# Kernel optimization log

Measured on AMD Instinct MI355X. Metric: run time of the kernel, lower is better.

## Reference

```python
import jax, jax.numpy as jnp
import numpy as np

D_MODEL = 1024
H = 16
D_K = D_MODEL // H
B, S = 1, 4096


def setup_inputs() -> dict:
    key = jax.random.key(0)
    ks = jax.random.split(key, 12)
    std = 1.0 / np.sqrt(D_MODEL)
    inp = {
        "q": jax.random.normal(ks[0], (B, S, D_MODEL), dtype=jnp.float32),
        "k": jax.random.normal(ks[1], (B, S, D_MODEL), dtype=jnp.float32),
        "v": jax.random.normal(ks[2], (B, S, D_MODEL), dtype=jnp.float32),
        "mask": jax.random.randint(ks[3], (B, 1, S, S), 0, 2).astype(bool),
        # nn.Linear params (torch convention: y = x @ W.T + b), weights [out, in]
        "wq": jax.random.uniform(ks[4], (D_MODEL, D_MODEL), jnp.float32, -std, std),
        "bq": jax.random.uniform(ks[5], (D_MODEL,), jnp.float32, -std, std),
        "wk": jax.random.uniform(ks[6], (D_MODEL, D_MODEL), jnp.float32, -std, std),
        "bk": jax.random.uniform(ks[7], (D_MODEL,), jnp.float32, -std, std),
        "wv": jax.random.uniform(ks[8], (D_MODEL, D_MODEL), jnp.float32, -std, std),
        "bv": jax.random.uniform(ks[9], (D_MODEL,), jnp.float32, -std, std),
        "wo": jax.random.uniform(ks[10], (D_MODEL, D_MODEL), jnp.float32, -std, std),
        "bo": jax.random.uniform(ks[11], (D_MODEL,), jnp.float32, -std, std),
    }
    return inp


def _split_heads(x):
    # [b, s, (h d)] -> [b, h, s, d]
    b, s, _ = x.shape
    return x.reshape(b, s, H, D_K).transpose(0, 2, 1, 3)


def reference(q, k, v, mask, wq, bq, wk, bk, wv, bv, wo, bo):
    b, s, d = q.shape
    qh = _split_heads(q @ wq.T + bq)
    kh = _split_heads(k @ wk.T + bk)
    vh = _split_heads(v @ wv.T + bv)
    # NOTE: original scales by sqrt(d_model), not sqrt(d_k) — keep faithful.
    score = jnp.einsum("bhqd,bhkd->bhqk", qh, kh) / jnp.sqrt(jnp.float32(d))
    score = jnp.where(mask, jnp.float32(-1e9), score)
    attn = jax.nn.softmax(score, axis=-1)  # dropout is identity in eval mode
    wv_out = jnp.einsum("bhqk,bhkd->bhqd", attn, vh)
    concat = wv_out.transpose(0, 2, 1, 3).reshape(b, s, d)
    return concat @ wo.T + bo
```

## Files before the change

### kernel.cpp

```cpp
#include <hip/hip_runtime.h>
#include <hip/hip_bf16.h>
#include <math.h>

typedef __attribute__((ext_vector_type(4))) float f32x4;
typedef __attribute__((ext_vector_type(8))) short s16x8;
typedef __attribute__((ext_vector_type(4))) short s16x4;

#define S_LEN 4096
#define DMODEL 1024
#define NHEADS 16
#define DHEAD 64

__device__ __forceinline__ unsigned short f2bf(float f) {
  union { float f; unsigned int u; } x; x.f = f;
  return (unsigned short)((x.u + 0x7FFFu + ((x.u >> 16) & 1u)) >> 16);
}

__device__ __forceinline__ float fexp2(float x) {
#if __has_builtin(__builtin_amdgcn_exp2f)
  return __builtin_amdgcn_exp2f(x);
#else
  float r; asm("v_exp_f32 %0, %1" : "=v"(r) : "v"(x)); return r;
#endif
}

__device__ __forceinline__ void gload_lds16(const void* g, void* l) {
  __builtin_amdgcn_global_load_lds(
      (const __attribute__((address_space(1))) unsigned int*)g,
      (__attribute__((address_space(3))) unsigned int*)l, 16, 0, 0);
}

__global__ __launch_bounds__(256) void mask_lane(const int* __restrict__ mask,
                                                 unsigned long long* __restrict__ lmask) {
  const int qg = blockIdx.x;
  const int wv = threadIdx.x >> 6, l = threadIdx.x & 63;
  const int lr = l & 15, lg = l >> 4;
  const int* base = mask + (size_t)(qg * 16 + lr) * S_LEN;
  for (int t = wv; t < 64; t += 4) {
#pragma unroll
    for (int kg = 0; kg < 4; ++kg) {
#pragma unroll
      for (int j = 0; j < 4; ++j) {
        unsigned long long b = __ballot(base[t * 64 + kg * 16 + lg * 4 + j] != 0);
        if (l == 0) lmask[((size_t)qg * 64 + t) * 16 + kg * 4 + j] = b;
      }
    }
  }
}

__global__ __launch_bounds__(256) void cast_bf16(
    const float* __restrict__ s0, const float* __restrict__ s1, const float* __restrict__ s2,
    const float* __restrict__ s3, const float* __restrict__ s4, const float* __restrict__ s5,
    const float* __restrict__ s6, unsigned short* __restrict__ dst) {
  const int z = blockIdx.y;
  const float* src = (z == 0) ? s0 : (z == 1) ? s1 : (z == 2) ? s2 :
                     (z == 3) ? s3 : (z == 4) ? s4 : (z == 5) ? s5 : s6;
  const int n = (z < 3) ? (S_LEN * DMODEL) : (DMODEL * DMODEL);
  unsigned short* d = dst + ((z < 3) ? (size_t)z * S_LEN * DMODEL
                                     : (size_t)3 * S_LEN * DMODEL + (size_t)(z - 3) * DMODEL * DMODEL);
  const int i = (blockIdx.x * 256 + threadIdx.x) * 4;
  if (i < n) {
    f32x4 v = *(const f32x4*)(src + i);
    s16x4 o;
#pragma unroll
    for (int j = 0; j < 4; ++j) o[j] = (short)f2bf(v[j]);
    *(s16x4*)(d + i) = o;
  }
}

template<int OUT_MODE>
__device__ __forceinline__ void gemm_b16_body(const unsigned short* __restrict__ A,
                                              const unsigned short* __restrict__ W,
                                              const float* __restrict__ bias,
                                              void* __restrict__ outp, float scale) {
  constexpr int K = DMODEL, N = DMODEL, M = S_LEN;
  constexpr int BM = 128, BK = 32;
  __shared__ unsigned short Alds[BM * BK];
  __shared__ unsigned short Blds[BM * BK];
  const int tid = threadIdx.x;
  const int l = tid & 63, wid = tid >> 6;
  const int lr = l & 15, lg = l >> 4;
  const int bm = blockIdx.x * BM, bn = blockIdx.y * BM;
  const int wm = (wid >> 1) * 64, wn = (wid & 1) * 64;

  const int srow = tid >> 2;
  const int schunk = (tid & 3) ^ (srow & 3);
  const unsigned short* As = A + (size_t)(bm + srow) * K + schunk * 8;
  const unsigned short* Ws = W + (size_t)(bn + srow) * K + schunk * 8;
  unsigned short* Ald = &Alds[srow * BK + (tid & 3) * 8];
  unsigned short* Bld = &Blds[srow * BK + (tid & 3) * 8];

  f32x4 acc[4][4] = {};
  const int xc = (lg ^ (lr & 3)) * 8;

  for (int k0 = 0; k0 < K; k0 += BK) {
    __syncthreads();
    gload_lds16(As + k0, Ald);
    gload_lds16(As + (size_t)64 * K + k0, Ald + 64 * BK);
    gload_lds16(Ws + k0, Bld);
    gload_lds16(Ws + (size_t)64 * K + k0, Bld + 64 * BK);
    __syncthreads();

    s16x8 af[4], bfr[4];
#pragma unroll
    for (int mi = 0; mi < 4; ++mi)
      af[mi] = *(const s16x8*)&Alds[(wm + mi * 16 + lr) * BK + xc];
#pragma unroll
    for (int ni = 0; ni < 4; ++ni)
      bfr[ni] = *(const s16x8*)&Blds[(wn + ni * 16 + lr) * BK + xc];
#pragma unroll
    for (int mi = 0; mi < 4; ++mi)
#pragma unroll
      for (int ni = 0; ni < 4; ++ni)
        acc[mi][ni] = __builtin_amdgcn_mfma_f32_16x16x32_bf16(af[mi], bfr[ni], acc[mi][ni], 0, 0, 0);
  }

#pragma unroll
  for (int ni = 0; ni < 4; ++ni) {
    const int n = bn + wn + ni * 16 + lr;
    const float bv = bias[n];
#pragma unroll
    for (int mi = 0; mi < 4; ++mi) {
#pragma unroll
      for (int j = 0; j < 4; ++j) {
        const int m = bm + wm + mi * 16 + lg * 4 + j;
        const float val = (acc[mi][ni][j] + bv) * scale;
        if constexpr (OUT_MODE == 1) {
          unsigned short* out = (unsigned short*)outp;
          out[((size_t)(n >> 6) * M + m) * DHEAD + (n & 63)] = f2bf(val);
        } else if constexpr (OUT_MODE == 2) {
          unsigned short* out = (unsigned short*)outp;
          out[((size_t)(n >> 6) * DHEAD + (n & 63)) * M + m] = f2bf(val);
        } else {
          float* out = (float*)outp;
          out[(size_t)m * N + n] = val;
        }
      }
    }
  }
}

template<int A_BF16, int OUT_MODE>
__device__ __forceinline__ void gemm_f32_body(const void* __restrict__ Ap,
                                              const float* __restrict__ W,
                                              const float* __restrict__ bias,
                                              void* __restrict__ outp, float scale) {
  constexpr int K = DMODEL, N = DMODEL, M = S_LEN;
  constexpr int BM = 128, BK = 32, LDT = 40;
  __shared__ unsigned short Alds[BM * LDT];
  __shared__ unsigned short Blds[BM * LDT];
  const int tid = threadIdx.x;
  const int l = tid & 63, wid = tid >> 6;
  const int lr = l & 15, lg = l >> 4;
  const int bm = blockIdx.x * BM;
  const int bn = blockIdx.y * BM;
  const int wm = (wid >> 1) * 64, wn = (wid & 1) * 64;

  f32x4 acc[4][4] = {};

  for (int k0 = 0; k0 < K; k0 += BK) {
    __syncthreads();
    if constexpr (A_BF16) {
      const unsigned short* A = (const unsigned short*)Ap;
      const int col = (tid & 3) * 8, row = tid >> 2;
#pragma unroll
      for (int p = 0; p < 2; ++p) {
        const int r = row + p * 64;
        *(s16x8*)&Alds[r * LDT + col] =
            *(const s16x8*)(A + (size_t)(bm + r) * K + k0 + col);
      }
    } else {
      const float* A = (const float*)Ap;
      const int col = (tid & 7) * 4, row = tid >> 3;
#pragma unroll
      for (int p = 0; p < 4; ++p) {
        const int r = row + p * 32;
        f32x4 vv = *(const f32x4*)(A + (size_t)(bm + r) * K + k0 + col);
        s16x4 o;
#pragma unroll
        for (int j = 0; j < 4; ++j) o[j] = (short)f2bf(vv[j]);
        *(s16x4*)&Alds[r * LDT + col] = o;
      }
    }
    {
      const float* Wf = W;
      const int col = (tid & 7) * 4, row = tid >> 3;
#pragma unroll
      for (int p = 0; p < 4; ++p) {
        const int r = row + p * 32;
        f32x4 vv = *(const f32x4*)(Wf + (size_t)(bn + r) * K + k0 + col);
        s16x4 o;
#pragma unroll
        for (int j = 0; j < 4; ++j) o[j] = (short)f2bf(vv[j]);
        *(s16x4*)&Blds[r * LDT + col] = o;
      }
    }
    __syncthreads();
    s16x8 af[4], bfr[4];
#pragma unroll
    for (int mi = 0; mi < 4; ++mi)
      af[mi] = *(const s16x8*)&Alds[(wm + mi * 16 + lr) * LDT + lg * 8];
#pragma unroll
    for (int ni = 0; ni < 4; ++ni)
      bfr[ni] = *(const s16x8*)&Blds[(wn + ni * 16 + lr) * LDT + lg * 8];
#pragma unroll
    for (int mi = 0; mi < 4; ++mi)
#pragma unroll
      for (int ni = 0; ni < 4; ++ni)
        acc[mi][ni] = __builtin_amdgcn_mfma_f32_16x16x32_bf16(af[mi], bfr[ni], acc[mi][ni], 0, 0, 0);
  }

#pragma unroll
  for (int ni = 0; ni < 4; ++ni) {
    const int n = bn + wn + ni * 16 + lr;
    const float bv = bias[n];
#pragma unroll
    for (int mi = 0; mi < 4; ++mi) {
#pragma unroll
      for (int j = 0; j < 4; ++j) {
        const int m = bm + wm + mi * 16 + lg * 4 + j;
        const float val = (acc[mi][ni][j] + bv) * scale;
        if constexpr (OUT_MODE == 1) {
          unsigned short* out = (unsigned short*)outp;
          out[((size_t)(n >> 6) * M + m) * DHEAD + (n & 63)] = f2bf(val);
        } else if constexpr (OUT_MODE == 2) {
          unsigned short* out = (unsigned short*)outp;
          out[((size_t)(n >> 6) * DHEAD + (n & 63)) * M + m] = f2bf(val);
        } else {
          float* out = (float*)outp;
          out[(size_t)m * N + n] = val;
        }
      }
    }
  }
}

#define QSCALE 0.04508422f

__global__ __launch_bounds__(256) void proj_qkv_b16(
    const unsigned short* __restrict__ qb, const unsigned short* __restrict__ kb,
    const unsigned short* __restrict__ vb,
    const unsigned short* __restrict__ wqb, const float* __restrict__ bq,
    const unsigned short* __restrict__ wkb, const float* __restrict__ bk,
    const unsigned short* __restrict__ wvb, const float* __restrict__ bv,
    unsigned short* __restrict__ ws) {
  const int z = blockIdx.z;
  if (z == 0)      gemm_b16_body<1>(qb, wqb, bq, ws, QSCALE);
  else if (z == 1) gemm_b16_body<1>(kb, wkb, bk, ws + (size_t)S_LEN * DMODEL, 1.0f);
  else             gemm_b16_body<2>(vb, wvb, bv, ws + (size_t)2 * S_LEN * DMODEL, 1.0f);
}
__global__ __launch_bounds__(256) void outproj_b16(
    const unsigned short* __restrict__ concat, const unsigned short* __restrict__ wob,
    const float* __restrict__ bo, float* __restrict__ out) {
  gemm_b16_body<0>(concat, wob, bo, out, 1.0f);
}
__global__ __launch_bounds__(256) void proj_qkv_f32(
    const float* __restrict__ q, const float* __restrict__ k, const float* __restrict__ v,
    const float* __restrict__ wq, const float* __restrict__ bq,
    const float* __restrict__ wk, const float* __restrict__ bk,
    const float* __restrict__ wv, const float* __restrict__ bv,
    unsigned short* __restrict__ ws) {
  const int z = blockIdx.z;
  if (z == 0)      gemm_f32_body<0, 1>(q, wq, bq, ws, QSCALE);
  else if (z == 1) gemm_f32_body<0, 1>(k, wk, bk, ws + (size_t)S_LEN * DMODEL, 1.0f);
  else             gemm_f32_body<0, 2>(v, wv, bv, ws + (size_t)2 * S_LEN * DMODEL, 1.0f);
}
__global__ __launch_bounds__(256) void outproj_f32(
    const unsigned short* __restrict__ concat, const float* __restrict__ wo,
    const float* __restrict__ bo, float* __restrict__ out) {
  gemm_f32_body<1, 0>(concat, wo, bo, out, 1.0f);
}

template<int NSPLIT>
__global__ __launch_bounds__(512, 4) void attn_fwd(
    const unsigned short* __restrict__ Qh, const unsigned short* __restrict__ Kh,
    const unsigned short* __restrict__ Vt, const unsigned long long* __restrict__ lmask,
    unsigned short* __restrict__ outp,
    float* __restrict__ lpart) {
  __shared__ unsigned short Klds[2][64 * 64];
  __shared__ unsigned short Vlds[2][64 * 64];
  __shared__ unsigned short P_lds[8][32][76];

  const int tid = threadIdx.x;
  const int l = tid & 63, wid = tid >> 6;
  const int lr = l & 15, lg = l >> 4;
  const int per = 32 * NSPLIT;
  const int swz = (blockIdx.x & 7) * per + (blockIdx.x >> 3);
  const int h = swz / (16 * NSPLIT);
  const int split = (NSPLIT == 2) ? ((swz >> 4) & 1) : 0;
  const int qb = swz & 15;
  const int qrow0 = qb * 256 + wid * 32;
  const int kv0 = split * (S_LEN / NSPLIT);
  constexpr int NT = (S_LEN / NSPLIT) / 64;
  const int T0 = kv0 >> 6;

  const unsigned short* Qbase = Qh + ((size_t)h * S_LEN + qrow0) * DHEAD;
  s16x8 qf[2][2];
#pragma unroll
  for (int sub = 0; sub < 2; ++sub)
#pragma unroll
    for (int ds = 0; ds < 2; ++ds)
      qf[sub][ds] = *(const s16x8*)(Qbase + (sub * 16 + lr) * DHEAD + ds * 32 + lg * 8);

  const int wid_u = __builtin_amdgcn_readfirstlane(wid);
  const int qg0 = qb * 16 + wid_u * 2;
  const unsigned long long* mq0 = lmask + (size_t)qg0 * 64 * 16;
  const unsigned long long* mq1 = mq0 + (size_t)64 * 16;

  const int srow = l >> 3;
  const int schunk = (l & 7) ^ srow;
  const unsigned short* Kst = Kh + (size_t)h * S_LEN * DHEAD
                              + (size_t)(kv0 + wid * 8 + srow) * DHEAD + schunk * 8;
  const unsigned short* Vst = Vt + (size_t)h * DHEAD * S_LEN
                              + (size_t)(wid * 8 + srow) * S_LEN + kv0 + schunk * 8;
  const int sdst = (wid * 8) * 64;

  f32x4 o_acc[2][4] = {};
  float lsum[2] = {0.f, 0.f};

  gload_lds16(Kst, &Klds[0][sdst]);
  gload_lds16(Vst, &Vlds[0][sdst]);
  __syncthreads();

  const int xr = lr & 7;

  for (int t = 0; t < NT; ++t) {
    const int buf = t & 1;
    if (t < NT - 1) {
      gload_lds16(Kst + (size_t)(t + 1) * 64 * DHEAD, &Klds[buf ^ 1][sdst]);
      gload_lds16(Vst + (t + 1) * 64, &Vlds[buf ^ 1][sdst]);
    }

    const unsigned short* Kb = &Klds[buf][0];
    f32x4 sc[2][4];
    __builtin_amdgcn_s_setprio(1);
#pragma unroll
    for (int kg = 0; kg < 4; ++kg) {
      const int r = kg * 16 + lr;
      s16x8 k0 = *(const s16x8*)(Kb + r * 64 + ((lg ^ xr) * 8));
      s16x8 k1 = *(const s16x8*)(Kb + r * 64 + (((lg + 4) ^ xr) * 8));
#pragma unroll
      for (int sub = 0; sub < 2; ++sub) {
        f32x4 z = {};
        z = __builtin_amdgcn_mfma_f32_16x16x32_bf16(k0, qf[sub][0], z, 0, 0, 0);
        sc[sub][kg] = __builtin_amdgcn_mfma_f32_16x16x32_bf16(k1, qf[sub][1], z, 0, 0, 0);
      }
    }
    __builtin_amdgcn_s_setprio(0);

    const size_t mo = (size_t)(T0 + t) * 16;
#pragma unroll
    for (int sub = 0; sub < 2; ++sub) {
      const unsigned long long* qp = (sub ? mq1 : mq0) + mo;
#pragma unroll
      for (int kg = 0; kg < 4; ++kg) {
        float p[4];
#pragma unroll
        for (int j = 0; j < 4; ++j) {
          const unsigned long long mw = qp[kg * 4 + j];
          float pv = fexp2(sc[sub][kg][j]);
          asm("v_cndmask_b32 %0, %1, 0, %2" : "=v"(pv) : "v"(pv), "s"(mw));
          p[j] = pv;
          lsum[sub] += pv;
        }
        unsigned int w0, w1;
        asm("v_cvt_pk_bf16_f32 %0, %1, %2" : "=v"(w0) : "v"(p[0]), "v"(p[1]));
        asm("v_cvt_pk_bf16_f32 %0, %1, %2" : "=v"(w1) : "v"(p[2]), "v"(p[3]));
        uint2 pk; pk.x = w0; pk.y = w1;
        *(uint2*)&P_lds[wid][sub * 16 + lr][kg * 16 + lg * 4] = pk;
      }
    }
    asm volatile("s_waitcnt lgkmcnt(0)" ::: "memory");
    __builtin_amdgcn_sched_barrier(0);

    s16x8 pf[2][2];
#pragma unroll
    for (int sub = 0; sub < 2; ++sub)
#pragma unroll
      for (int ks = 0; ks < 2; ++ks)
        pf[sub][ks] = *(const s16x8*)&P_lds[wid][sub * 16 + lr][ks * 32 + lg * 8];

    const unsigned short* Vb = &Vlds[buf][0];
    __builtin_amdgcn_s_setprio(1);
#pragma unroll
    for (int dg = 0; dg < 4; ++dg) {
      const int r = dg * 16 + lr;
      s16x8 v0 = *(const s16x8*)(Vb + r * 64 + ((lg ^ xr) * 8));
      s16x8 v1 = *(const s16x8*)(Vb + r * 64 + (((lg + 4) ^ xr) * 8));
#pragma unroll
      for (int sub = 0; sub < 2; ++sub) {
        o_acc[sub][dg] = __builtin_amdgcn_mfma_f32_16x16x32_bf16(pf[sub][0], v0, o_acc[sub][dg], 0, 0, 0);
        o_acc[sub][dg] = __builtin_amdgcn_mfma_f32_16x16x32_bf16(pf[sub][1], v1, o_acc[sub][dg], 0, 0, 0);
      }
    }
    __builtin_amdgcn_s_setprio(0);

    __syncthreads();
  }

#pragma unroll
  for (int sub = 0; sub < 2; ++sub) {
    lsum[sub] += __shfl_xor(lsum[sub], 16, 64);
    lsum[sub] += __shfl_xor(lsum[sub], 32, 64);
  }

  if constexpr (NSPLIT == 2) {
    unsigned short* op = outp + ((size_t)(split * NHEADS + h) * S_LEN) * DHEAD;
#pragma unroll
    for (int sub = 0; sub < 2; ++sub)
#pragma unroll
      for (int dg = 0; dg < 4; ++dg)
#pragma unroll
        for (int j = 0; j < 4; ++j) {
          const int q = qrow0 + sub * 16 + lg * 4 + j;
          op[(size_t)q * DHEAD + dg * 16 + lr] = f2bf(o_acc[sub][dg][j]);
        }
    if (l < 16) {
      float* lp = lpart + (size_t)(split * NHEADS + h) * S_LEN + qrow0;
      lp[lr] = lsum[0];
      lp[16 + lr] = lsum[1];
    }
  } else {
    float rs[2][4];
#pragma unroll
    for (int sub = 0; sub < 2; ++sub)
#pragma unroll
      for (int j = 0; j < 4; ++j)
        rs[sub][j] = __shfl(lsum[sub], lg * 4 + j, 64);
#pragma unroll
    for (int sub = 0; sub < 2; ++sub)
#pragma unroll
      for (int dg = 0; dg < 4; ++dg)
#pragma unroll
        for (int j = 0; j < 4; ++j) {
          const int q = qrow0 + sub * 16 + lg * 4 + j;
          outp[(size_t)q * DMODEL + h * DHEAD + dg * 16 + lr] =
              f2bf(o_acc[sub][dg][j] / rs[sub][j]);
        }
  }
}

__global__ __launch_bounds__(256) void attn_combine(
    const unsigned short* __restrict__ opart, const float* __restrict__ lpart,
    unsigned short* __restrict__ concat) {
  const int idx = blockIdx.x * 256 + threadIdx.x;
  const int d4 = (idx & 15) * 4;
  const int hq = idx >> 4;
  const int h = hq >> 12, q = hq & 4095;
  const size_t o0 = ((size_t)h * S_LEN + q) * DHEAD + d4;
  const size_t o1 = o0 + (size_t)NHEADS * S_LEN * DHEAD;
  const float linv = 1.0f / (lpart[(size_t)h * S_LEN + q] +
                             lpart[(size_t)(NHEADS + h) * S_LEN + q]);
  s16x4 a = *(const s16x4*)(opart + o0);
  s16x4 b = *(const s16x4*)(opart + o1);
  s16x4 r;
#pragma unroll
  for (int i = 0; i < 4; ++i) {
    union { unsigned int u; float f; } xa, xb;
    xa.u = ((unsigned int)(unsigned short)a[i]) << 16;
    xb.u = ((unsigned int)(unsigned short)b[i]) << 16;
    r[i] = (short)f2bf((xa.f + xb.f) * linv);
  }
  *(s16x4*)(concat + ((size_t)q * DMODEL + h * DHEAD + d4)) = r;
}

extern "C" void kernel_launch(void* const* d_in, const int* in_sizes, int n_in,
                              void* d_out, int out_size, void* d_ws, size_t ws_size,
                              hipStream_t stream) {
  const float* q  = (const float*)d_in[0];
  const float* k  = (const float*)d_in[1];
  const float* v  = (const float*)d_in[2];
  const int* mask = (const int*)d_in[3];
  const float* wq = (const float*)d_in[4];
  const float* bq = (const float*)d_in[5];
  const float* wk = (const float*)d_in[6];
  const float* bk = (const float*)d_in[7];
  const float* wv = (const float*)d_in[8];
  const float* bv = (const float*)d_in[9];
  const float* wo = (const float*)d_in[10];
  const float* bo = (const float*)d_in[11];
  float* out = (float*)d_out;

  const size_t SD = (size_t)S_LEN * DMODEL, DD = (size_t)DMODEL * DMODEL;
  unsigned short* wsq = (unsigned short*)d_ws;
  unsigned short* wsc = wsq + 3 * SD;
  unsigned long long* wslm = (unsigned long long*)(wsc + SD);
  unsigned short* cast0 = (unsigned short*)(wslm + (size_t)256 * 64 * 16);
  const size_t need = (size_t)((char*)(cast0 + 3 * SD + 4 * DD) - (char*)d_ws);
  const bool big = ws_size >= need;

  mask_lane<<<dim3(256), dim3(256), 0, stream>>>(mask, wslm);

  if (big) {
    unsigned short* qb  = cast0;
    unsigned short* kb  = qb + SD;
    unsigned short* vb  = kb + SD;
    unsigned short* wqb = vb + SD;
    unsigned short* wkb = wqb + DD;
    unsigned short* wvb = wkb + DD;
    unsigned short* wob = wvb + DD;
    unsigned short* opart = cast0;
    float* lpart = (float*)vb;
    cast_bf16<<<dim3(4096, 7), dim3(256), 0, stream>>>(q, k, v, wq, wk, wv, wo, cast0);
    proj_qkv_b16<<<dim3(32, 8, 3), dim3(256), 0, stream>>>(qb, kb, vb, wqb, bq, wkb, bk, wvb, bv, wsq);
    attn_fwd<2><<<dim3(512), dim3(512), 0, stream>>>(wsq, wsq + SD, wsq + 2 * SD, wslm, opart, lpart);
    attn_combine<<<dim3(4096), dim3(256), 0, stream>>>(opart, lpart, wsc);
    outproj_b16<<<dim3(32, 8), dim3(256), 0, stream>>>(wsc, wob, bo, out);
  } else {
    proj_qkv_f32<<<dim3(32, 8, 3), dim3(256), 0, stream>>>(q, k, v, wq, bq, wk, bk, wv, bv, wsq);
    attn_fwd<1><<<dim3(256), dim3(512), 0, stream>>>(wsq, wsq + SD, wsq + 2 * SD, wslm, wsc, nullptr);
    outproj_f32<<<dim3(32, 8), dim3(256), 0, stream>>>(wsc, wo, bo, out);
  }
}
```

Before: 219.1 us.

## Double-buffer bf16 GEMM LDS tiles and widen mask_lane grid

```diff
diff --git a/kernel.cpp b/kernel.cpp
--- a/kernel.cpp
+++ b/kernel.cpp
@@ -33,17 +33,15 @@
 __global__ __launch_bounds__(256) void mask_lane(const int* __restrict__ mask,
                                                  unsigned long long* __restrict__ lmask) {
   const int qg = blockIdx.x;
-  const int wv = threadIdx.x >> 6, l = threadIdx.x & 63;
-  const int lr = l & 15, lg = l >> 4;
-  const int* base = mask + (size_t)(qg * 16 + lr) * S_LEN;
-  for (int t = wv; t < 64; t += 4) {
-#pragma unroll
-    for (int kg = 0; kg < 4; ++kg) {
-#pragma unroll
-      for (int j = 0; j < 4; ++j) {
-        unsigned long long b = __ballot(base[t * 64 + kg * 16 + lg * 4 + j] != 0);
-        if (l == 0) lmask[((size_t)qg * 64 + t) * 16 + kg * 4 + j] = b;
-      }
+  const int t = blockIdx.y * 4 + (threadIdx.x >> 6);
+  const int l = threadIdx.x & 63, lr = l & 15, lg = l >> 4;
+  const int* base = mask + (size_t)(qg * 16 + lr) * S_LEN + t * 64;
+#pragma unroll
+  for (int kg = 0; kg < 4; ++kg) {
+#pragma unroll
+    for (int j = 0; j < 4; ++j) {
+      unsigned long long b = __ballot(base[kg * 16 + lg * 4 + j] != 0);
+      if (l == 0) lmask[((size_t)qg * 64 + t) * 16 + kg * 4 + j] = b;
     }
   }
 }
@@ -74,9 +72,9 @@
                                               const float* __restrict__ bias,
                                               void* __restrict__ outp, float scale) {
   constexpr int K = DMODEL, N = DMODEL, M = S_LEN;
-  constexpr int BM = 128, BK = 32;
-  __shared__ unsigned short Alds[BM * BK];
-  __shared__ unsigned short Blds[BM * BK];
+  constexpr int BM = 128, BK = 32, NT = K / BK;
+  __shared__ unsigned short Alds[2][BM * BK];
+  __shared__ unsigned short Blds[2][BM * BK];
   const int tid = threadIdx.x;
   const int l = tid & 63, wid = tid >> 6;
   const int lr = l & 15, lg = l >> 4;
@@ -87,32 +85,43 @@
   const int schunk = (tid & 3) ^ (srow & 3);
   const unsigned short* As = A + (size_t)(bm + srow) * K + schunk * 8;
   const unsigned short* Ws = W + (size_t)(bn + srow) * K + schunk * 8;
-  unsigned short* Ald = &Alds[srow * BK + (tid & 3) * 8];
-  unsigned short* Bld = &Blds[srow * BK + (tid & 3) * 8];
+  const int ldoff = srow * BK + (tid & 3) * 8;
 
   f32x4 acc[4][4] = {};
   const int xc = (lg ^ (lr & 3)) * 8;
 
-  for (int k0 = 0; k0 < K; k0 += BK) {
-    __syncthreads();
-    gload_lds16(As + k0, Ald);
-    gload_lds16(As + (size_t)64 * K + k0, Ald + 64 * BK);
-    gload_lds16(Ws + k0, Bld);
-    gload_lds16(Ws + (size_t)64 * K + k0, Bld + 64 * BK);
-    __syncthreads();
+  gload_lds16(As, &Alds[0][ldoff]);
+  gload_lds16(As + (size_t)64 * K, &Alds[0][ldoff + 64 * BK]);
+  gload_lds16(Ws, &Blds[0][ldoff]);
+  gload_lds16(Ws + (size_t)64 * K, &Blds[0][ldoff + 64 * BK]);
+  __syncthreads();
+
+  for (int t = 0; t < NT; ++t) {
+    const int buf = t & 1;
+    if (t < NT - 1) {
+      const int k0 = (t + 1) * BK;
+      gload_lds16(As + k0, &Alds[buf ^ 1][ldoff]);
+      gload_lds16(As + (size_t)64 * K + k0, &Alds[buf ^ 1][ldoff + 64 * BK]);
+      gload_lds16(Ws + k0, &Blds[buf ^ 1][ldoff]);
+      gload_lds16(Ws + (size_t)64 * K + k0, &Blds[buf ^ 1][ldoff + 64 * BK]);
+    }
 
     s16x8 af[4], bfr[4];
 #pragma unroll
     for (int mi = 0; mi < 4; ++mi)
-      af[mi] = *(const s16x8*)&Alds[(wm + mi * 16 + lr) * BK + xc];
+      af[mi] = *(const s16x8*)&Alds[buf][(wm + mi * 16 + lr) * BK + xc];
 #pragma unroll
     for (int ni = 0; ni < 4; ++ni)
-      bfr[ni] = *(const s16x8*)&Blds[(wn + ni * 16 + lr) * BK + xc];
+      bfr[ni] = *(const s16x8*)&Blds[buf][(wn + ni * 16 + lr) * BK + xc];
+    __builtin_amdgcn_s_setprio(1);
 #pragma unroll
     for (int mi = 0; mi < 4; ++mi)
 #pragma unroll
       for (int ni = 0; ni < 4; ++ni)
         acc[mi][ni] = __builtin_amdgcn_mfma_f32_16x16x32_bf16(af[mi], bfr[ni], acc[mi][ni], 0, 0, 0);
+    __builtin_amdgcn_s_setprio(0);
+
+    __syncthreads();
   }
 
 #pragma unroll
@@ -183,12 +192,11 @@
       }
     }
     {
-      const float* Wf = W;
       const int col = (tid & 7) * 4, row = tid >> 3;
 #pragma unroll
       for (int p = 0; p < 4; ++p) {
         const int r = row + p * 32;
-        f32x4 vv = *(const f32x4*)(Wf + (size_t)(bn + r) * K + k0 + col);
+        f32x4 vv = *(const f32x4*)(W + (size_t)(bn + r) * K + k0 + col);
         s16x4 o;
 #pragma unroll
         for (int j = 0; j < 4; ++j) o[j] = (short)f2bf(vv[j]);
@@ -489,7 +497,7 @@
   const size_t need = (size_t)((char*)(cast0 + 3 * SD + 4 * DD) - (char*)d_ws);
   const bool big = ws_size >= need;
 
-  mask_lane<<<dim3(256), dim3(256), 0, stream>>>(mask, wslm);
+  mask_lane<<<dim3(256, 16), dim3(256), 0, stream>>>(mask, wslm);
 
   if (big) {
     unsigned short* qb  = cast0;
```

Measured after the change: 218.9 us. Within noise of the previous version (-0.1%).
